# Kernel tuning notes

Hardware: AMD Instinct MI355X
Metric: run time of the kernel (lower is better)

The kernel has to match this reference:

```python
import jax, jax.numpy as jnp
import numpy as np

WINDOW = 5  # must be odd so conv 'same' output length == tlength


def setup_inputs() -> dict:
    key = jax.random.key(0)
    tlength = 16777216
    return {"factor": jax.random.normal(key, (tlength,), dtype=jnp.float32)}


def reference(factor):
    window = WINDOW
    # moving average: conv1d with ones kernel, padding=window//2 (== 'same' for odd window)
    w = jnp.ones((window,), dtype=factor.dtype)
    moving_average = jnp.convolve(factor, w, mode='same') / window
    # rate of change: 0 followed by squared consecutive differences
    diffs = (moving_average[:-1] - moving_average[1:]) ** 2
    change = jnp.concatenate([jnp.zeros((1,), dtype=factor.dtype), diffs])
    change = change / jnp.sum(change)
    # power-weighted elementwise scaling
    return (1.0 - change) ** 5 * factor
```

## Files before the change

kernel.cpp:

```cpp
#include <hip/hip_runtime.h>


#define BLOCK 256
#define GRID_CAP 1024
#define NSUB 32
#define SUB_STRIDE 16

typedef __attribute__((ext_vector_type(4))) float vfloat4;

__device__ unsigned int g_sub[NSUB * SUB_STRIDE];
__device__ unsigned int g_stage2 = 0u;
__device__ unsigned int g_go = 0u;
__device__ float g_partials[GRID_CAP];

__device__ __forceinline__ float change_term(const float* __restrict__ f, long long i, long long n) {
    if (i < 1) return 0.0f;
    float a = (i >= 3)    ? f[i - 3] : 0.0f;
    float b = (i + 2 < n) ? f[i + 2] : 0.0f;
    float d = a - b;
    return d * d;
}

__device__ __forceinline__ float pow5(float t) {
    float t2 = t * t;
    float t4 = t2 * t2;
    return t4 * t;
}

__device__ __forceinline__ float vec_terms(float4 p, float4 c, float4 q) {
    float d0 = p.y - c.z;
    float d1 = p.z - c.w;
    float d2 = p.w - q.x;
    float d3 = c.x - q.y;
    return d0 * d0 + d1 * d1 + d2 * d2 + d3 * d3;
}

__device__ __forceinline__ vfloat4 vec_out(float4 p, float4 c, float4 q, float inv) {
    float d0 = p.y - c.z;
    float d1 = p.z - c.w;
    float d2 = p.w - q.x;
    float d3 = c.x - q.y;
    vfloat4 o;
    o.x = pow5(1.0f - d0 * d0 * inv) * c.x;
    o.y = pow5(1.0f - d1 * d1 * inv) * c.y;
    o.z = pow5(1.0f - d2 * d2 * inv) * c.z;
    o.w = pow5(1.0f - d3 * d3 * inv) * c.w;
    return o;
}

__global__ __launch_bounds__(BLOCK)
void fused_onepass(const float* __restrict__ f, int nvec, long long n,
                   float* __restrict__ out) {
    const float4* __restrict__ fv = (const float4*)f;
    vfloat4* __restrict__ ov = (vfloat4*)out;
    const int grid = (int)gridDim.x;
    const int T = grid * BLOCK;
    const int tid = blockIdx.x * BLOCK + threadIdx.x;
    const int M = nvec - 2;

    float acc = 0.0f;
    int idx = tid;
    for (; idx + 3 * T < M; idx += 4 * T) {
        float4 p[4], c[4], q[4];
        #pragma unroll
        for (int u = 0; u < 4; ++u) {
            int v = 1 + idx + u * T;
            p[u] = fv[v - 1];
            c[u] = fv[v];
            q[u] = fv[v + 1];
        }
        #pragma unroll
        for (int u = 0; u < 4; ++u)
            acc += vec_terms(p[u], c[u], q[u]);
    }
    for (; idx < M; idx += T) {
        int v = 1 + idx;
        acc += vec_terms(fv[v - 1], fv[v], fv[v + 1]);
    }
    if (tid == 0) {
        #pragma unroll
        for (int k = 0; k < 4; ++k) acc += change_term(f, k, n);
        long long j0 = n - 4;
        #pragma unroll
        for (int k = 0; k < 4; ++k) acc += change_term(f, j0 + k, n);
    }

    #pragma unroll
    for (int off = 32; off > 0; off >>= 1)
        acc += __shfl_down(acc, off, 64);
    __shared__ float smem[4];
    __shared__ float s_stot;
    __shared__ int s_timeout;
    const int lane = threadIdx.x & 63;
    const int wave = threadIdx.x >> 6;
    if (lane == 0) smem[wave] = acc;
    __syncthreads();

    if (threadIdx.x == 0) {
        float bp = smem[0] + smem[1] + smem[2] + smem[3];
        __hip_atomic_store(&g_partials[blockIdx.x], bp,
                           __ATOMIC_RELAXED, __HIP_MEMORY_SCOPE_SYSTEM);
        __builtin_amdgcn_s_waitcnt(0);

        const unsigned per = (unsigned)grid / NSUB;
        unsigned old = __hip_atomic_fetch_add(&g_sub[(blockIdx.x & (NSUB - 1)) * SUB_STRIDE],
                                              1u, __ATOMIC_RELAXED, __HIP_MEMORY_SCOPE_SYSTEM);
        unsigned gen = old / per;
        if (old - gen * per == per - 1u) {
            unsigned old2 = __hip_atomic_fetch_add(&g_stage2, 1u,
                                __ATOMIC_RELAXED, __HIP_MEMORY_SCOPE_SYSTEM);
            if ((old2 % NSUB) == NSUB - 1u)
                __hip_atomic_fetch_add(&g_go, 1u,
                    __ATOMIC_RELAXED, __HIP_MEMORY_SCOPE_SYSTEM);
        }

        const unsigned want = gen + 1u;
        int timeout = 0;
        long long polls = 0;
        while (__hip_atomic_load(&g_go, __ATOMIC_RELAXED,
                                 __HIP_MEMORY_SCOPE_SYSTEM) < want) {
            __builtin_amdgcn_s_sleep(8);
            if (++polls > (200LL << 10)) { timeout = 1; break; }
        }
        s_timeout = timeout;
    }
    __syncthreads();

    float s = 0.0f;
    if (!s_timeout) {
        for (int k = threadIdx.x; k < grid; k += BLOCK)
            s += __hip_atomic_load(&g_partials[k], __ATOMIC_RELAXED,
                                   __HIP_MEMORY_SCOPE_SYSTEM);
    } else {
        for (int v = 1 + (int)threadIdx.x; v < 1 + M; v += BLOCK)
            s += vec_terms(fv[v - 1], fv[v], fv[v + 1]);
        if (threadIdx.x == 0) {
            #pragma unroll
            for (int k = 0; k < 4; ++k) s += change_term(f, k, n);
            long long j0 = n - 4;
            #pragma unroll
            for (int k = 0; k < 4; ++k) s += change_term(f, j0 + k, n);
        }
    }
    #pragma unroll
    for (int off = 32; off > 0; off >>= 1)
        s += __shfl_down(s, off, 64);
    if (lane == 0) smem[wave] = s;
    __syncthreads();
    if (threadIdx.x == 0) s_stot = smem[0] + smem[1] + smem[2] + smem[3];
    __syncthreads();
    const float inv = 1.0f / s_stot;

    idx = tid;
    for (; idx + 3 * T < M; idx += 4 * T) {
        float4 p[4], c[4], q[4];
        #pragma unroll
        for (int u = 0; u < 4; ++u) {
            int v = 1 + idx + u * T;
            p[u] = fv[v - 1];
            c[u] = fv[v];
            q[u] = fv[v + 1];
        }
        #pragma unroll
        for (int u = 0; u < 4; ++u)
            __builtin_nontemporal_store(vec_out(p[u], c[u], q[u], inv),
                                        &ov[1 + idx + u * T]);
    }
    for (; idx < M; idx += T) {
        int v = 1 + idx;
        __builtin_nontemporal_store(vec_out(fv[v - 1], fv[v], fv[v + 1], inv), &ov[v]);
    }
    if (tid == 0) {
        #pragma unroll
        for (int k = 0; k < 4; ++k) {
            float cge = change_term(f, k, n) * inv;
            out[k] = pow5(1.0f - cge) * f[k];
        }
        long long j0 = n - 4;
        #pragma unroll
        for (int k = 0; k < 4; ++k) {
            long long j = j0 + k;
            float cge = change_term(f, j, n) * inv;
            out[j] = pow5(1.0f - cge) * f[j];
        }
    }
}

extern "C" void kernel_launch(void* const* d_in, const int* in_sizes, int n_in,
                              void* d_out, int out_size, void* d_ws, size_t ws_size,
                              hipStream_t stream) {
    const float* f = (const float*)d_in[0];
    float* out = (float*)d_out;
    long long n = (long long)in_sizes[0];
    int nvec = (int)(n / 4);
    (void)d_ws; (void)ws_size;

    static int grid = -1;
    if (grid < 0) {
        int dev = 0;
        (void)hipGetDevice(&dev);
        int ncu = 0;
        if (hipDeviceGetAttribute(&ncu, hipDeviceAttributeMultiprocessorCount, dev) != hipSuccess || ncu <= 0)
            ncu = 256;
        int bpc = 0;
        if (hipOccupancyMaxActiveBlocksPerMultiprocessor(&bpc, (const void*)fused_onepass, BLOCK, 0) != hipSuccess
            || bpc <= 0)
            bpc = 2;
        long long g = (long long)bpc * ncu;
        if (g > GRID_CAP) g = GRID_CAP;
        g -= g % NSUB;
        if (g < NSUB) g = NSUB;
        grid = (int)g;
    }

    fused_onepass<<<grid, BLOCK, 0, stream>>>(f, nvec, n, out);
}
```

Baseline: 131.8 us.

## Carry squared differences in registers across grid barrier to avoid reloading neighbors

Adds a register-carry kernel with a fixed grid of 2048 blocks, each thread owning 8 float4 vectors. The squared differences computed in the reduction pass stay in registers across the grid-wide barrier, so the output pass only reloads the center vector instead of three neighbors. A fallback dynamic-grid kernel is kept for when occupancy is too low to make all blocks co-resident. The costs are higher register pressure, a tree barrier widened to 64 sub-counters, and reliance on 8 blocks per CU being resident so the spin barrier does not stall.

```diff
diff --git a/kernel.cpp b/kernel.cpp
--- a/kernel.cpp
+++ b/kernel.cpp
@@ -2,8 +2,9 @@
 
 
 #define BLOCK 256
-#define GRID_CAP 1024
-#define NSUB 32
+#define RGRID 2048
+#define VPT 8
+#define NSUB 64
 #define SUB_STRIDE 16
 
 typedef __attribute__((ext_vector_type(4))) float vfloat4;
@@ -11,7 +12,7 @@
 __device__ unsigned int g_sub[NSUB * SUB_STRIDE];
 __device__ unsigned int g_stage2 = 0u;
 __device__ unsigned int g_go = 0u;
-__device__ float g_partials[GRID_CAP];
+__device__ float g_partials[RGRID];
 
 __device__ __forceinline__ float change_term(const float* __restrict__ f, long long i, long long n) {
     if (i < 1) return 0.0f;
@@ -48,34 +49,62 @@
     return o;
 }
 
-__global__ __launch_bounds__(BLOCK)
-void fused_onepass(const float* __restrict__ f, int nvec, long long n,
-                   float* __restrict__ out) {
+__device__ __forceinline__ int barrier_arrive_wait(int bid, int grid, float bp) {
+    __hip_atomic_store(&g_partials[bid], bp,
+                       __ATOMIC_RELAXED, __HIP_MEMORY_SCOPE_SYSTEM);
+    __builtin_amdgcn_s_waitcnt(0);
+
+    const unsigned per = (unsigned)grid / NSUB;
+    unsigned old = __hip_atomic_fetch_add(&g_sub[(bid & (NSUB - 1)) * SUB_STRIDE],
+                                          1u, __ATOMIC_RELAXED, __HIP_MEMORY_SCOPE_SYSTEM);
+    unsigned gen = old / per;
+    if (old - gen * per == per - 1u) {
+        unsigned old2 = __hip_atomic_fetch_add(&g_stage2, 1u,
+                            __ATOMIC_RELAXED, __HIP_MEMORY_SCOPE_SYSTEM);
+        if ((old2 % NSUB) == NSUB - 1u)
+            __hip_atomic_fetch_add(&g_go, 1u,
+                __ATOMIC_RELAXED, __HIP_MEMORY_SCOPE_SYSTEM);
+    }
+    const unsigned want = gen + 1u;
+    long long polls = 0;
+    while (__hip_atomic_load(&g_go, __ATOMIC_RELAXED,
+                             __HIP_MEMORY_SCOPE_SYSTEM) < want) {
+        __builtin_amdgcn_s_sleep(8);
+        if (++polls > (200LL << 10)) return 1;
+    }
+    return 0;
+}
+
+
+__global__ __launch_bounds__(BLOCK, 8)
+void fused_regcarry(const float* __restrict__ f, int nvec, long long n,
+                    float* __restrict__ out) {
     const float4* __restrict__ fv = (const float4*)f;
     vfloat4* __restrict__ ov = (vfloat4*)out;
-    const int grid = (int)gridDim.x;
-    const int T = grid * BLOCK;
+    const int T = RGRID * BLOCK;
     const int tid = blockIdx.x * BLOCK + threadIdx.x;
     const int M = nvec - 2;
 
+    float4 d2[VPT];
     float acc = 0.0f;
-    int idx = tid;
-    for (; idx + 3 * T < M; idx += 4 * T) {
-        float4 p[4], c[4], q[4];
-        #pragma unroll
-        for (int u = 0; u < 4; ++u) {
-            int v = 1 + idx + u * T;
-            p[u] = fv[v - 1];
-            c[u] = fv[v];
-            q[u] = fv[v + 1];
-        }
-        #pragma unroll
-        for (int u = 0; u < 4; ++u)
-            acc += vec_terms(p[u], c[u], q[u]);
-    }
-    for (; idx < M; idx += T) {
-        int v = 1 + idx;
-        acc += vec_terms(fv[v - 1], fv[v], fv[v + 1]);
+    #pragma unroll
+    for (int k = 0; k < VPT; ++k) {
+        int idx = tid + k * T;
+        if (idx < M) {
+            int v = 1 + idx;
+            float4 p = fv[v - 1], c = fv[v], q = fv[v + 1];
+            float e0 = p.y - c.z;
+            float e1 = p.z - c.w;
+            float e2 = p.w - q.x;
+            float e3 = c.x - q.y;
+            d2[k].x = e0 * e0;
+            d2[k].y = e1 * e1;
+            d2[k].z = e2 * e2;
+            d2[k].w = e3 * e3;
+            acc += d2[k].x + d2[k].y + d2[k].z + d2[k].w;
+        } else {
+            d2[k].x = d2[k].y = d2[k].z = d2[k].w = 0.0f;
+        }
     }
     if (tid == 0) {
         #pragma unroll
@@ -96,34 +125,118 @@
     if (lane == 0) smem[wave] = acc;
     __syncthreads();
 
-    if (threadIdx.x == 0) {
-        float bp = smem[0] + smem[1] + smem[2] + smem[3];
-        __hip_atomic_store(&g_partials[blockIdx.x], bp,
-                           __ATOMIC_RELAXED, __HIP_MEMORY_SCOPE_SYSTEM);
-        __builtin_amdgcn_s_waitcnt(0);
-
-        const unsigned per = (unsigned)grid / NSUB;
-        unsigned old = __hip_atomic_fetch_add(&g_sub[(blockIdx.x & (NSUB - 1)) * SUB_STRIDE],
-                                              1u, __ATOMIC_RELAXED, __HIP_MEMORY_SCOPE_SYSTEM);
-        unsigned gen = old / per;
-        if (old - gen * per == per - 1u) {
-            unsigned old2 = __hip_atomic_fetch_add(&g_stage2, 1u,
-                                __ATOMIC_RELAXED, __HIP_MEMORY_SCOPE_SYSTEM);
-            if ((old2 % NSUB) == NSUB - 1u)
-                __hip_atomic_fetch_add(&g_go, 1u,
-                    __ATOMIC_RELAXED, __HIP_MEMORY_SCOPE_SYSTEM);
-        }
-
-        const unsigned want = gen + 1u;
-        int timeout = 0;
-        long long polls = 0;
-        while (__hip_atomic_load(&g_go, __ATOMIC_RELAXED,
-                                 __HIP_MEMORY_SCOPE_SYSTEM) < want) {
-            __builtin_amdgcn_s_sleep(8);
-            if (++polls > (200LL << 10)) { timeout = 1; break; }
-        }
-        s_timeout = timeout;
-    }
+    if (threadIdx.x == 0)
+        s_timeout = barrier_arrive_wait(blockIdx.x, RGRID,
+                                        smem[0] + smem[1] + smem[2] + smem[3]);
+    __syncthreads();
+
+    float s = 0.0f;
+    if (!s_timeout) {
+        for (int k = threadIdx.x; k < RGRID; k += BLOCK)
+            s += __hip_atomic_load(&g_partials[k], __ATOMIC_RELAXED,
+                                   __HIP_MEMORY_SCOPE_SYSTEM);
+    } else {
+        for (int v = 1 + (int)threadIdx.x; v < 1 + M; v += BLOCK)
+            s += vec_terms(fv[v - 1], fv[v], fv[v + 1]);
+        if (threadIdx.x == 0) {
+            #pragma unroll
+            for (int k = 0; k < 4; ++k) s += change_term(f, k, n);
+            long long j0 = n - 4;
+            #pragma unroll
+            for (int k = 0; k < 4; ++k) s += change_term(f, j0 + k, n);
+        }
+    }
+    #pragma unroll
+    for (int off = 32; off > 0; off >>= 1)
+        s += __shfl_down(s, off, 64);
+    if (lane == 0) smem[wave] = s;
+    __syncthreads();
+    if (threadIdx.x == 0) s_stot = smem[0] + smem[1] + smem[2] + smem[3];
+    __syncthreads();
+    const float inv = 1.0f / s_stot;
+
+    #pragma unroll
+    for (int k = 0; k < VPT; ++k) {
+        int idx = tid + k * T;
+        if (idx < M) {
+            int v = 1 + idx;
+            float4 c = fv[v];
+            vfloat4 o;
+            o.x = pow5(1.0f - d2[k].x * inv) * c.x;
+            o.y = pow5(1.0f - d2[k].y * inv) * c.y;
+            o.z = pow5(1.0f - d2[k].z * inv) * c.z;
+            o.w = pow5(1.0f - d2[k].w * inv) * c.w;
+            __builtin_nontemporal_store(o, &ov[v]);
+        }
+    }
+    if (tid == 0) {
+        #pragma unroll
+        for (int k = 0; k < 4; ++k) {
+            float cge = change_term(f, k, n) * inv;
+            out[k] = pow5(1.0f - cge) * f[k];
+        }
+        long long j0 = n - 4;
+        #pragma unroll
+        for (int k = 0; k < 4; ++k) {
+            long long j = j0 + k;
+            float cge = change_term(f, j, n) * inv;
+            out[j] = pow5(1.0f - cge) * f[j];
+        }
+    }
+}
+
+
+__global__ __launch_bounds__(BLOCK)
+void fused_dynamic(const float* __restrict__ f, int nvec, long long n,
+                   float* __restrict__ out) {
+    const float4* __restrict__ fv = (const float4*)f;
+    vfloat4* __restrict__ ov = (vfloat4*)out;
+    const int grid = (int)gridDim.x;
+    const int T = grid * BLOCK;
+    const int tid = blockIdx.x * BLOCK + threadIdx.x;
+    const int M = nvec - 2;
+
+    float acc = 0.0f;
+    int idx = tid;
+    for (; idx + 3 * T < M; idx += 4 * T) {
+        float4 p[4], c[4], q[4];
+        #pragma unroll
+        for (int u = 0; u < 4; ++u) {
+            int v = 1 + idx + u * T;
+            p[u] = fv[v - 1];
+            c[u] = fv[v];
+            q[u] = fv[v + 1];
+        }
+        #pragma unroll
+        for (int u = 0; u < 4; ++u)
+            acc += vec_terms(p[u], c[u], q[u]);
+    }
+    for (; idx < M; idx += T) {
+        int v = 1 + idx;
+        acc += vec_terms(fv[v - 1], fv[v], fv[v + 1]);
+    }
+    if (tid == 0) {
+        #pragma unroll
+        for (int k = 0; k < 4; ++k) acc += change_term(f, k, n);
+        long long j0 = n - 4;
+        #pragma unroll
+        for (int k = 0; k < 4; ++k) acc += change_term(f, j0 + k, n);
+    }
+
+    #pragma unroll
+    for (int off = 32; off > 0; off >>= 1)
+        acc += __shfl_down(acc, off, 64);
+    __shared__ float smem[4];
+    __shared__ float s_stot;
+    __shared__ int s_timeout;
+    const int lane = threadIdx.x & 63;
+    const int wave = threadIdx.x >> 6;
+    if (lane == 0) smem[wave] = acc;
+    __syncthreads();
+
+    if (threadIdx.x == 0)
+        s_timeout = barrier_arrive_wait(blockIdx.x, grid,
+                                        smem[0] + smem[1] + smem[2] + smem[3]);
     __syncthreads();
 
     float s = 0.0f;
@@ -195,23 +308,33 @@
     int nvec = (int)(n / 4);
     (void)d_ws; (void)ws_size;
 
-    static int grid = -1;
-    if (grid < 0) {
+    static int use_reg = -1;
+    static int dyn_grid = 0;
+    if (use_reg < 0) {
         int dev = 0;
         (void)hipGetDevice(&dev);
         int ncu = 0;
         if (hipDeviceGetAttribute(&ncu, hipDeviceAttributeMultiprocessorCount, dev) != hipSuccess || ncu <= 0)
             ncu = 256;
-        int bpc = 0;
-        if (hipOccupancyMaxActiveBlocksPerMultiprocessor(&bpc, (const void*)fused_onepass, BLOCK, 0) != hipSuccess
-            || bpc <= 0)
-            bpc = 2;
-        long long g = (long long)bpc * ncu;
-        if (g > GRID_CAP) g = GRID_CAP;
+        int bpc_reg = 0;
+        (void)hipOccupancyMaxActiveBlocksPerMultiprocessor(&bpc_reg, (const void*)fused_regcarry, BLOCK, 0);
+        long long M = (long long)nvec - 2;
+        bool cover = (long long)VPT * RGRID * BLOCK >= M;
+        use_reg = (bpc_reg * ncu >= RGRID && cover) ? 1 : 0;
+
+        int bpc_dyn = 0;
+        if (hipOccupancyMaxActiveBlocksPerMultiprocessor(&bpc_dyn, (const void*)fused_dynamic, BLOCK, 0) != hipSuccess
+            || bpc_dyn <= 0)
+            bpc_dyn = 2;
+        long long g = (long long)bpc_dyn * ncu;
+        if (g > RGRID) g = RGRID;
         g -= g % NSUB;
         if (g < NSUB) g = NSUB;
-        grid = (int)g;
-    }
-
-    fused_onepass<<<grid, BLOCK, 0, stream>>>(f, nvec, n, out);
-}
+        dyn_grid = (int)g;
+    }
+
+    if (use_reg)
+        fused_regcarry<<<RGRID, BLOCK, 0, stream>>>(f, nvec, n, out);
+    else
+        fused_dynamic<<<dyn_grid, BLOCK, 0, stream>>>(f, nvec, n, out);
+}
```

Result: no change. 130.1 us (-1.3%).
